# Kernel optimization log

Measured on AMD Instinct MI355X. Metric: run time of the kernel, lower is better.

The kernel has to match this reference:

```python
import jax, jax.numpy as jnp
import numpy as np

EPS = 1e-6
B, T, D = 8, 4096, 512


def setup_inputs() -> dict:
    key = jax.random.key(0)
    ks = jax.random.split(key, 8)
    s = 1.0 / np.sqrt(D)
    return {
        "summarization": jax.random.normal(ks[0], (B, D), jnp.float32),
        "decoder_output": jax.random.normal(ks[1], (B, T, D), jnp.float32),
        "W_hist": jax.random.normal(ks[2], (D, D), jnp.float32) * s,
        "b_hist": jnp.zeros((D,), jnp.float32),
        "W1": jax.random.normal(ks[3], (D, D), jnp.float32) * s,
        "W2": jax.random.normal(ks[4], (D, D), jnp.float32) * s,
        "W_out": jax.random.normal(ks[5], (D, D), jnp.float32) * s,
        "b_out": jnp.zeros((D,), jnp.float32),
        "gamma": jnp.ones((D,), jnp.float32),
        "beta": jnp.zeros((D,), jnp.float32),
    }


def reference(summarization, decoder_output, W_hist, b_hist, W1, W2, W_out, b_out, gamma, beta):
    # Causal running mean: equivalent to tril-mask bmm / row-count, but O(T).
    tgt_len = decoder_output.shape[1]
    counts = jnp.arange(1, tgt_len + 1, dtype=decoder_output.dtype)[None, :, None]
    history = jnp.cumsum(decoder_output, axis=1) / counts            # [B,T,D]
    history = jnp.tanh(history @ W_hist + b_hist)                    # history_linear + tanh
    # TransformMinus: linear1(summ) - linear2(history), then linear_out + tanh
    summ_proj = (summarization @ W1)[:, None, :]                     # [B,1,D] broadcasts over T
    out = summ_proj - history @ W2
    future = jnp.tanh(out @ W_out + b_out)
    # LayerPostprocessing (eval: dropout = identity): LayerNorm(future + decoder_output)
    x = future + decoder_output
    mu = jnp.mean(x, axis=-1, keepdims=True)
    var = jnp.mean(jnp.square(x - mu), axis=-1, keepdims=True)
    return (x - mu) / jnp.sqrt(var + EPS) * gamma + beta
```

## Files before the change

kernel.cpp:

```cpp
#include <hip/hip_runtime.h>
#include <hip/hip_bf16.h>
#include <stdint.h>
#include <stddef.h>

#define DEV static __device__ __forceinline__

typedef __attribute__((ext_vector_type(8))) short short8;
typedef __attribute__((ext_vector_type(4))) float floatx4;

constexpr int Tn = 4096, Dn = 512;
constexpr int NC = 128, CTm = 32;

union U8s { uint4 u4; unsigned short us[8]; };
union U4f { float4 f4; float f[4]; };
union U4s { uint2 u2; unsigned short us[4]; };

DEV float b2f(unsigned short u) {
  union { unsigned int i; float f; } c; c.i = ((unsigned int)u) << 16; return c.f;
}
DEV unsigned short f2b(float f) {
  union { float f; unsigned int u; } c; c.f = f;
  unsigned int r = c.u + 0x7fffu + ((c.u >> 16) & 1u);
  return (unsigned short)(r >> 16);
}
DEV float fast_tanh(float x) {
  float e = __expf(2.0f * x);
  return 1.0f - 2.0f / (e + 1.0f);
}

typedef __attribute__((address_space(1))) void GVOID;
typedef __attribute__((address_space(3))) void LVOID;
DEV void async16(const unsigned short* g, unsigned short* l) {
  __builtin_amdgcn_global_load_lds((GVOID*)g, (LVOID*)l, 16, 0, 0);
}

__global__ void k_scan_partial(const float* __restrict__ dec, float* __restrict__ part) {
  int idx = blockIdx.x * 256 + threadIdx.x;
  int d4 = idx & 127;
  int c  = (idx >> 7) & (NC - 1);
  int b  = idx >> 14;
  const float* p = dec + ((size_t)b * Tn + (size_t)c * CTm) * Dn + d4 * 4;
  float s[4] = {0,0,0,0};
#pragma unroll 4
  for (int i = 0; i < CTm; ++i) {
    U4f v; v.f4 = *(const float4*)(p + (size_t)i * Dn);
#pragma unroll
    for (int j = 0; j < 4; ++j) s[j] += v.f[j];
  }
  float* o = part + ((size_t)(b * NC + c)) * Dn + d4 * 4;
#pragma unroll
  for (int j = 0; j < 4; ++j) o[j] = s[j];
}

__global__ void k_scan_apply(const float* __restrict__ dec,
                             const float* __restrict__ part,
                             unsigned short* __restrict__ M) {
  int idx = blockIdx.x * 256 + threadIdx.x;
  int d8 = idx & 63;
  int c  = (idx >> 6) & (NC - 1);
  int b  = idx >> 13;
  size_t rbase = (size_t)b * Tn + (size_t)c * CTm;
  float s[8] = {0,0,0,0,0,0,0,0};
  const float* pb = part + (size_t)b * NC * Dn + d8 * 8;
  for (int cc = 0; cc < c; ++cc) {
    U4f p0, p1;
    p0.f4 = *(const float4*)(pb + (size_t)cc * Dn);
    p1.f4 = *(const float4*)(pb + (size_t)cc * Dn + 4);
#pragma unroll
    for (int j = 0; j < 4; ++j) { s[j] += p0.f[j]; s[j + 4] += p1.f[j]; }
  }
  int t0 = c * CTm;
  for (int i = 0; i < CTm; ++i) {
    U4f v0, v1; U8s o;
    v0.f4 = *(const float4*)(dec + (rbase + i) * Dn + d8 * 8);
    v1.f4 = *(const float4*)(dec + (rbase + i) * Dn + d8 * 8 + 4);
    float inv = 1.0f / (float)(t0 + i + 1);
#pragma unroll
    for (int j = 0; j < 4; ++j) {
      s[j] += v0.f[j];     o.us[j]     = f2b(s[j] * inv);
      s[j + 4] += v1.f[j]; o.us[j + 4] = f2b(s[j + 4] * inv);
    }
    *(uint4*)(M + (rbase + i) * Dn + d8 * 8) = o.u4;
  }
}

__global__ void k_svec(const float* __restrict__ summ,
                       const unsigned short* __restrict__ W1WoT,
                       const float* __restrict__ bo,
                       float* __restrict__ spo) {
  int widx = blockIdx.x * 4 + (threadIdx.x >> 6);
  int lane = threadIdx.x & 63;
  int n = widx & 511; int b = widx >> 9;
  U8s w8; w8.u4 = *(const uint4*)(W1WoT + (size_t)n * Dn + lane * 8);
  U4f s0, s1;
  s0.f4 = *(const float4*)(summ + (size_t)b * Dn + lane * 8);
  s1.f4 = *(const float4*)(summ + (size_t)b * Dn + lane * 8 + 4);
  float acc = 0.f;
#pragma unroll
  for (int j = 0; j < 4; ++j) acc += s0.f[j] * b2f(w8.us[j]);
#pragma unroll
  for (int j = 0; j < 4; ++j) acc += s1.f[j] * b2f(w8.us[j + 4]);
#pragma unroll
  for (int o = 32; o > 0; o >>= 1) acc += __shfl_xor(acc, o, 64);
  if (lane == 0) spo[(size_t)b * Dn + n] = acc + bo[n];
}

__global__ void k_wprep(const float* __restrict__ Wh, const float* __restrict__ Wo,
                        const float* __restrict__ W1, const float* __restrict__ W2,
                        unsigned short* __restrict__ WhT, unsigned short* __restrict__ WoT,
                        unsigned short* __restrict__ W1b, unsigned short* __restrict__ W2b) {
  int blk = blockIdx.x;
  if (blk < 128) {
    const float* in = (blk < 64) ? Wh : Wo;
    unsigned short* out = (blk < 64) ? WhT : WoT;
    int lb = blk & 63;
    __shared__ float t[64][65];
    int n0 = (lb & 7) * 64, k0 = (lb >> 3) * 64;
#pragma unroll
    for (int l = 0; l < 16; ++l) {
      int lin = l * 256 + threadIdx.x;
      int r = lin >> 6, c = lin & 63;
      t[r][c] = in[(size_t)(k0 + r) * 512 + n0 + c];
    }
    __syncthreads();
#pragma unroll
    for (int l = 0; l < 16; ++l) {
      int lin = l * 256 + threadIdx.x;
      int r = lin >> 6, c = lin & 63;
      out[(size_t)(n0 + r) * 512 + k0 + c] = f2b(t[c][r]);
    }
  } else {
    const float* in = (blk < 160) ? W1 : W2;
    unsigned short* out = (blk < 160) ? W1b : W2b;
    int lb = (blk - 128) & 31;
    size_t base = ((size_t)lb * 256 + threadIdx.x) * 32;
#pragma unroll
    for (int l = 0; l < 8; ++l) {
      U4f v; v.f4 = *(const float4*)(in + base + l * 4);
      U4s o;
#pragma unroll
      for (int j = 0; j < 4; ++j) o.us[j] = f2b(v.f[j]);
      *(uint2*)(out + base + l * 4) = o.u2;
    }
  }
}

template<int EPI>
DEV void gemm_core(const unsigned short* __restrict__ A, const unsigned short* __restrict__ BT,
                   unsigned short* __restrict__ C, const float* __restrict__ bias,
                   const float* __restrict__ sproj, int m0, int n0) {
  __shared__ alignas(16) unsigned short sA[128 * 64];
  __shared__ alignas(16) unsigned short sB[128 * 64];
  const int tid  = threadIdx.x;
  const int lane = tid & 63;
  const int w    = tid >> 6;
  const int wm   = (w >> 1) * 64;
  const int wn   = (w & 1) * 64;
  const int rs   = lane & 15;
  const int quad = lane >> 4;

  floatx4 acc[4][4];
#pragma unroll
  for (int i = 0; i < 4; ++i)
#pragma unroll
    for (int j = 0; j < 4; ++j) acc[i][j] = (floatx4){0.f, 0.f, 0.f, 0.f};

  for (int kt = 0; kt < 512; kt += 64) {
#pragma unroll
    for (int l = 0; l < 4; ++l) {
      int ch = l * 256 + tid;
      int r = ch >> 3, kc = ch & 7;
      async16(A  + (size_t)(m0 + r) * 512 + kt + kc * 8, sA + (size_t)ch * 8);
      async16(BT + (size_t)(n0 + r) * 512 + kt + kc * 8, sB + (size_t)ch * 8);
    }
    asm volatile("s_waitcnt vmcnt(0)" ::: "memory");
    __syncthreads();

#pragma unroll
    for (int kk = 0; kk < 2; ++kk) {
      const int kb = kk * 32 + quad * 8;
      short8 af[4], bfr[4];
#pragma unroll
      for (int i = 0; i < 4; ++i)
        af[i] = *(const short8*)(sA + (size_t)(wm + i * 16 + rs) * 64 + kb);
#pragma unroll
      for (int j = 0; j < 4; ++j)
        bfr[j] = *(const short8*)(sB + (size_t)(wn + j * 16 + rs) * 64 + kb);
#pragma unroll
      for (int i = 0; i < 4; ++i)
#pragma unroll
        for (int j = 0; j < 4; ++j)
          acc[i][j] = __builtin_amdgcn_mfma_f32_16x16x32_bf16(af[i], bfr[j], acc[i][j], 0, 0, 0);
    }
    __syncthreads();
  }

#pragma unroll
  for (int i = 0; i < 4; ++i) {
#pragma unroll
    for (int j = 0; j < 4; ++j) {
      const int colg = n0 + wn + j * 16 + rs;
#pragma unroll
      for (int r = 0; r < 4; ++r) {
        const int rowg = m0 + wm + i * 16 + quad * 4 + r;
        float v = acc[i][j][r];
        if constexpr (EPI == 0)      v = fast_tanh(v + bias[colg]);
        else if constexpr (EPI == 3) v = fast_tanh(sproj[(rowg >> 12) * Dn + colg] - v);
        C[(size_t)rowg * 512 + colg] = f2b(v);
      }
    }
  }
}

template<int EPI>
__global__ __launch_bounds__(256, 2)
void k_gemm(const unsigned short* __restrict__ A, const unsigned short* __restrict__ BT,
            unsigned short* __restrict__ C, const float* __restrict__ bias,
            const float* __restrict__ sproj) {
  gemm_core<EPI>(A, BT, C, bias, sproj, blockIdx.x * 128, blockIdx.y * 128);
}

__global__ __launch_bounds__(256, 2)
void k_wgemm(const unsigned short* __restrict__ WoT,
             const unsigned short* __restrict__ W2b, const unsigned short* __restrict__ W1b,
             unsigned short* __restrict__ W2WoT, unsigned short* __restrict__ W1WoT) {
  const unsigned short* BT = blockIdx.z ? W1b : W2b;
  unsigned short* C = blockIdx.z ? W1WoT : W2WoT;
  gemm_core<2>(WoT, BT, C, nullptr, nullptr, blockIdx.x * 128, blockIdx.y * 128);
}

__global__ void k_ln(const unsigned short* __restrict__ F, const float* __restrict__ dec,
                     const float* __restrict__ gamma, const float* __restrict__ beta,
                     float* __restrict__ out) {
  int row  = blockIdx.x * 4 + (threadIdx.x >> 6);
  int lane = threadIdx.x & 63;
  size_t base = (size_t)row * Dn + lane * 8;
  U8s f8; f8.u4 = *(const uint4*)(F + base);
  U4f d0, d1; d0.f4 = *(const float4*)(dec + base); d1.f4 = *(const float4*)(dec + base + 4);
  float x[8]; float s = 0.f, sq = 0.f;
#pragma unroll
  for (int j = 0; j < 8; ++j) {
    float dv = (j < 4) ? d0.f[j] : d1.f[j - 4];
    x[j] = b2f(f8.us[j]) + dv; s += x[j]; sq += x[j] * x[j];
  }
#pragma unroll
  for (int o = 32; o > 0; o >>= 1) { s += __shfl_xor(s, o, 64); sq += __shfl_xor(sq, o, 64); }
  float mu   = s * (1.0f / 512.0f);
  float var  = sq * (1.0f / 512.0f) - mu * mu;
  float rstd = rsqrtf(var + 1e-6f);
  U4f g0, g1, b0, b1, o0, o1;
  g0.f4 = *(const float4*)(gamma + lane * 8); g1.f4 = *(const float4*)(gamma + lane * 8 + 4);
  b0.f4 = *(const float4*)(beta  + lane * 8); b1.f4 = *(const float4*)(beta  + lane * 8 + 4);
#pragma unroll
  for (int j = 0; j < 8; ++j) {
    float g = (j < 4) ? g0.f[j] : g1.f[j - 4];
    float b = (j < 4) ? b0.f[j] : b1.f[j - 4];
    float v = (x[j] - mu) * rstd * g + b;
    if (j < 4) o0.f[j] = v; else o1.f[j - 4] = v;
  }
  *(float4*)(out + base) = o0.f4;
  *(float4*)(out + base + 4) = o1.f4;
}

extern "C" void kernel_launch(void* const* d_in, const int* in_sizes, int n_in,
                              void* d_out, int out_size, void* d_ws, size_t ws_size,
                              hipStream_t stream) {
  (void)in_sizes; (void)n_in; (void)out_size; (void)ws_size;
  const float* summ = (const float*)d_in[0];
  const float* dec  = (const float*)d_in[1];
  const float* Wh   = (const float*)d_in[2];
  const float* bh   = (const float*)d_in[3];
  const float* W1   = (const float*)d_in[4];
  const float* W2   = (const float*)d_in[5];
  const float* Wo   = (const float*)d_in[6];
  const float* bo   = (const float*)d_in[7];
  const float* gam  = (const float*)d_in[8];
  const float* bet  = (const float*)d_in[9];
  float* out = (float*)d_out;

  char* ws = (char*)d_ws;
  unsigned short* Mbuf  = (unsigned short*)(ws);
  unsigned short* Hbuf  = (unsigned short*)(ws + 33554432);
  float*          part  = (float*)(ws + 67108864);
  float*          spo   = (float*)(ws + 69206016);
  unsigned short* WhT   = (unsigned short*)(ws + 69238784);
  unsigned short* WoT   = (unsigned short*)(ws + 69763072);
  unsigned short* W2b   = (unsigned short*)(ws + 70287360);
  unsigned short* W2WoT = (unsigned short*)(ws + 70811648);
  unsigned short* W1b   = (unsigned short*)(ws + 71335936);
  unsigned short* W1WoT = (unsigned short*)(ws + 71860224);

  k_scan_partial<<<512, 256, 0, stream>>>(dec, part);

  k_wprep<<<192, 256, 0, stream>>>(Wh, Wo, W1, W2, WhT, WoT, W1b, W2b);
  k_wgemm<<<dim3(4, 4, 2), 256, 0, stream>>>(WoT, W2b, W1b, W2WoT, W1WoT);

  k_svec<<<1024, 256, 0, stream>>>(summ, W1WoT, bo, spo);

  k_scan_apply<<<256, 256, 0, stream>>>(dec, part, Mbuf);

  k_gemm<0><<<dim3(256, 4), 256, 0, stream>>>(Mbuf, WhT, Hbuf, bh, nullptr);
  k_gemm<3><<<dim3(256, 4), 256, 0, stream>>>(Hbuf, W2WoT, Mbuf, nullptr, spo);

  k_ln<<<8192, 256, 0, stream>>>(Mbuf, dec, gam, bet, out);
}
```

Baseline: 265.4 us.

## Fuse second GEMM with LayerNorm and add parallel chunk-prefix kernel for scan

The second GEMM now computes full 512-column rows per block (64x512 tile). Its epilogue applies tanh and the residual add, reduces mean and variance across waves through LDS, and writes the normalized fp32 output directly. This removes the separate LayerNorm kernel and the bf16 round-trip of the intermediate buffer. Separately, a new k_prefix kernel does an in-LDS Hillis-Steele scan of the chunk partial sums, so k_scan_apply reads one precomputed prefix instead of re-summing all earlier chunks, and it runs with more threads. The trade-off is that the fused GEMM uses a large (~72KB) LDS tile with no double buffering, which may limit occupancy and leave memory latency exposed.

```diff
diff --git a/kernel.cpp b/kernel.cpp
--- a/kernel.cpp
+++ b/kernel.cpp
@@ -52,35 +52,62 @@
   for (int j = 0; j < 4; ++j) o[j] = s[j];
 }
 
+__global__ void k_prefix(const float* __restrict__ part, float* __restrict__ P) {
+  int b = blockIdx.x >> 3, dg = blockIdx.x & 7;
+  __shared__ float S[NC * 64];
+  const float* src = part + (size_t)b * NC * Dn + dg * 64;
+#pragma unroll
+  for (int l = 0; l < 32; ++l) {
+    int lin = l * 256 + threadIdx.x;
+    int c = lin >> 6, d = lin & 63;
+    S[c * 64 + d] = src[(size_t)c * Dn + d];
+  }
+  __syncthreads();
+  for (int off = 1; off < NC; off <<= 1) {
+    float t[32];
+#pragma unroll
+    for (int l = 0; l < 32; ++l) {
+      int lin = l * 256 + threadIdx.x;
+      int c = lin >> 6, d = lin & 63;
+      t[l] = (c >= off) ? S[(c - off) * 64 + d] : 0.f;
+    }
+    __syncthreads();
+#pragma unroll
+    for (int l = 0; l < 32; ++l) {
+      int lin = l * 256 + threadIdx.x;
+      int c = lin >> 6, d = lin & 63;
+      S[c * 64 + d] += t[l];
+    }
+    __syncthreads();
+  }
+  float* dst = P + (size_t)b * NC * Dn + dg * 64;
+#pragma unroll
+  for (int l = 0; l < 32; ++l) {
+    int lin = l * 256 + threadIdx.x;
+    int c = lin >> 6, d = lin & 63;
+    dst[(size_t)c * Dn + d] = (c > 0) ? S[(c - 1) * 64 + d] : 0.f;
+  }
+}
+
 __global__ void k_scan_apply(const float* __restrict__ dec,
-                             const float* __restrict__ part,
+                             const float* __restrict__ P,
                              unsigned short* __restrict__ M) {
   int idx = blockIdx.x * 256 + threadIdx.x;
-  int d8 = idx & 63;
-  int c  = (idx >> 6) & (NC - 1);
-  int b  = idx >> 13;
+  int d4 = idx & 127;
+  int c  = (idx >> 7) & (NC - 1);
+  int b  = idx >> 14;
   size_t rbase = (size_t)b * Tn + (size_t)c * CTm;
-  float s[8] = {0,0,0,0,0,0,0,0};
-  const float* pb = part + (size_t)b * NC * Dn + d8 * 8;
-  for (int cc = 0; cc < c; ++cc) {
-    U4f p0, p1;
-    p0.f4 = *(const float4*)(pb + (size_t)cc * Dn);
-    p1.f4 = *(const float4*)(pb + (size_t)cc * Dn + 4);
-#pragma unroll
-    for (int j = 0; j < 4; ++j) { s[j] += p0.f[j]; s[j + 4] += p1.f[j]; }
-  }
+  U4f pv; pv.f4 = *(const float4*)(P + ((size_t)(b * NC + c)) * Dn + d4 * 4);
+  float s[4] = {pv.f[0], pv.f[1], pv.f[2], pv.f[3]};
   int t0 = c * CTm;
+#pragma unroll 4
   for (int i = 0; i < CTm; ++i) {
-    U4f v0, v1; U8s o;
-    v0.f4 = *(const float4*)(dec + (rbase + i) * Dn + d8 * 8);
-    v1.f4 = *(const float4*)(dec + (rbase + i) * Dn + d8 * 8 + 4);
+    U4f v; v.f4 = *(const float4*)(dec + (rbase + i) * Dn + d4 * 4);
+    U4s o;
     float inv = 1.0f / (float)(t0 + i + 1);
 #pragma unroll
-    for (int j = 0; j < 4; ++j) {
-      s[j] += v0.f[j];     o.us[j]     = f2b(s[j] * inv);
-      s[j + 4] += v1.f[j]; o.us[j + 4] = f2b(s[j + 4] * inv);
-    }
-    *(uint4*)(M + (rbase + i) * Dn + d8 * 8) = o.u4;
+    for (int j = 0; j < 4; ++j) { s[j] += v.f[j]; o.us[j] = f2b(s[j] * inv); }
+    *(uint2*)(M + (rbase + i) * Dn + d4 * 4) = o.u2;
   }
 }
 
@@ -148,7 +175,7 @@
 template<int EPI>
 DEV void gemm_core(const unsigned short* __restrict__ A, const unsigned short* __restrict__ BT,
                    unsigned short* __restrict__ C, const float* __restrict__ bias,
-                   const float* __restrict__ sproj, int m0, int n0) {
+                   int m0, int n0) {
   __shared__ alignas(16) unsigned short sA[128 * 64];
   __shared__ alignas(16) unsigned short sB[128 * 64];
   const int tid  = threadIdx.x;
@@ -204,8 +231,7 @@
       for (int r = 0; r < 4; ++r) {
         const int rowg = m0 + wm + i * 16 + quad * 4 + r;
         float v = acc[i][j][r];
-        if constexpr (EPI == 0)      v = fast_tanh(v + bias[colg]);
-        else if constexpr (EPI == 3) v = fast_tanh(sproj[(rowg >> 12) * Dn + colg] - v);
+        if constexpr (EPI == 0) v = fast_tanh(v + bias[colg]);
         C[(size_t)rowg * 512 + colg] = f2b(v);
       }
     }
@@ -215,9 +241,8 @@
 template<int EPI>
 __global__ __launch_bounds__(256, 2)
 void k_gemm(const unsigned short* __restrict__ A, const unsigned short* __restrict__ BT,
-            unsigned short* __restrict__ C, const float* __restrict__ bias,
-            const float* __restrict__ sproj) {
-  gemm_core<EPI>(A, BT, C, bias, sproj, blockIdx.x * 128, blockIdx.y * 128);
+            unsigned short* __restrict__ C, const float* __restrict__ bias) {
+  gemm_core<EPI>(A, BT, C, bias, blockIdx.x * 128, blockIdx.y * 128);
 }
 
 __global__ __launch_bounds__(256, 2)
@@ -226,40 +251,138 @@
              unsigned short* __restrict__ W2WoT, unsigned short* __restrict__ W1WoT) {
   const unsigned short* BT = blockIdx.z ? W1b : W2b;
   unsigned short* C = blockIdx.z ? W1WoT : W2WoT;
-  gemm_core<2>(WoT, BT, C, nullptr, nullptr, blockIdx.x * 128, blockIdx.y * 128);
-}
-
-__global__ void k_ln(const unsigned short* __restrict__ F, const float* __restrict__ dec,
-                     const float* __restrict__ gamma, const float* __restrict__ beta,
-                     float* __restrict__ out) {
-  int row  = blockIdx.x * 4 + (threadIdx.x >> 6);
-  int lane = threadIdx.x & 63;
-  size_t base = (size_t)row * Dn + lane * 8;
-  U8s f8; f8.u4 = *(const uint4*)(F + base);
-  U4f d0, d1; d0.f4 = *(const float4*)(dec + base); d1.f4 = *(const float4*)(dec + base + 4);
-  float x[8]; float s = 0.f, sq = 0.f;
-#pragma unroll
-  for (int j = 0; j < 8; ++j) {
-    float dv = (j < 4) ? d0.f[j] : d1.f[j - 4];
-    x[j] = b2f(f8.us[j]) + dv; s += x[j]; sq += x[j] * x[j];
-  }
-#pragma unroll
-  for (int o = 32; o > 0; o >>= 1) { s += __shfl_xor(s, o, 64); sq += __shfl_xor(sq, o, 64); }
-  float mu   = s * (1.0f / 512.0f);
-  float var  = sq * (1.0f / 512.0f) - mu * mu;
-  float rstd = rsqrtf(var + 1e-6f);
-  U4f g0, g1, b0, b1, o0, o1;
-  g0.f4 = *(const float4*)(gamma + lane * 8); g1.f4 = *(const float4*)(gamma + lane * 8 + 4);
-  b0.f4 = *(const float4*)(beta  + lane * 8); b1.f4 = *(const float4*)(beta  + lane * 8 + 4);
-#pragma unroll
-  for (int j = 0; j < 8; ++j) {
-    float g = (j < 4) ? g0.f[j] : g1.f[j - 4];
-    float b = (j < 4) ? b0.f[j] : b1.f[j - 4];
-    float v = (x[j] - mu) * rstd * g + b;
-    if (j < 4) o0.f[j] = v; else o1.f[j - 4] = v;
-  }
-  *(float4*)(out + base) = o0.f4;
-  *(float4*)(out + base + 4) = o1.f4;
+  gemm_core<2>(WoT, BT, C, nullptr, blockIdx.x * 128, blockIdx.y * 128);
+}
+
+__global__ __launch_bounds__(512, 4)
+void k_gemm2ln(const unsigned short* __restrict__ H, const unsigned short* __restrict__ BT,
+               const float* __restrict__ spo, const float* __restrict__ dec,
+               const float* __restrict__ gamma, const float* __restrict__ beta,
+               float* __restrict__ out) {
+  __shared__ alignas(16) unsigned short sA[64 * 64];
+  __shared__ alignas(16) unsigned short sB[512 * 64];
+  const int tid  = threadIdx.x;
+  const int lane = tid & 63;
+  const int cg   = tid >> 6;
+  const int m0   = blockIdx.x * 64;
+  const int b    = blockIdx.x >> 6;
+  const int rs   = lane & 15;
+  const int quad = lane >> 4;
+
+  floatx4 acc[4][4];
+#pragma unroll
+  for (int i = 0; i < 4; ++i)
+#pragma unroll
+    for (int j = 0; j < 4; ++j) acc[i][j] = (floatx4){0.f, 0.f, 0.f, 0.f};
+
+  for (int kt = 0; kt < 512; kt += 64) {
+    {
+      int r = tid >> 3, kc = tid & 7;
+      async16(H + (size_t)(m0 + r) * 512 + kt + kc * 8, sA + (size_t)tid * 8);
+    }
+#pragma unroll
+    for (int l = 0; l < 8; ++l) {
+      int ch = l * 512 + tid;
+      int r = ch >> 3, kc = ch & 7;
+      async16(BT + (size_t)r * 512 + kt + kc * 8, sB + (size_t)ch * 8);
+    }
+    asm volatile("s_waitcnt vmcnt(0)" ::: "memory");
+    __syncthreads();
+
+#pragma unroll
+    for (int kk = 0; kk < 2; ++kk) {
+      const int kb = kk * 32 + quad * 8;
+      short8 af[4], bfr[4];
+#pragma unroll
+      for (int i = 0; i < 4; ++i)
+        af[i] = *(const short8*)(sA + (size_t)(i * 16 + rs) * 64 + kb);
+#pragma unroll
+      for (int j = 0; j < 4; ++j)
+        bfr[j] = *(const short8*)(sB + (size_t)(cg * 64 + j * 16 + rs) * 64 + kb);
+#pragma unroll
+      for (int i = 0; i < 4; ++i)
+#pragma unroll
+        for (int j = 0; j < 4; ++j)
+          acc[i][j] = __builtin_amdgcn_mfma_f32_16x16x32_bf16(af[i], bfr[j], acc[i][j], 0, 0, 0);
+    }
+    __syncthreads();
+  }
+
+  float* redS = (float*)sA;
+  float* redQ = redS + 512;
+  float* muL  = redQ + 512;
+  float* rsL  = muL + 64;
+
+  float spo_v[4], gam_v[4], bet_v[4];
+#pragma unroll
+  for (int j = 0; j < 4; ++j) {
+    int col = cg * 64 + j * 16 + rs;
+    spo_v[j] = spo[(size_t)b * 512 + col];
+    gam_v[j] = gamma[col];
+    bet_v[j] = beta[col];
+  }
+
+  float ps[4][4], ps2[4][4];
+#pragma unroll
+  for (int i = 0; i < 4; ++i)
+#pragma unroll
+    for (int r = 0; r < 4; ++r) { ps[i][r] = 0.f; ps2[i][r] = 0.f; }
+
+#pragma unroll
+  for (int i = 0; i < 4; ++i)
+#pragma unroll
+    for (int j = 0; j < 4; ++j) {
+      const int colg = cg * 64 + j * 16 + rs;
+#pragma unroll
+      for (int r = 0; r < 4; ++r) {
+        const int rowg = m0 + i * 16 + quad * 4 + r;
+        float x = fast_tanh(spo_v[j] - acc[i][j][r]) + dec[(size_t)rowg * 512 + colg];
+        acc[i][j][r] = x;
+        ps[i][r] += x; ps2[i][r] += x * x;
+      }
+    }
+#pragma unroll
+  for (int off = 1; off < 16; off <<= 1)
+#pragma unroll
+    for (int i = 0; i < 4; ++i)
+#pragma unroll
+      for (int r = 0; r < 4; ++r) {
+        ps[i][r]  += __shfl_xor(ps[i][r],  off, 64);
+        ps2[i][r] += __shfl_xor(ps2[i][r], off, 64);
+      }
+  if (rs == 0) {
+#pragma unroll
+    for (int i = 0; i < 4; ++i)
+#pragma unroll
+      for (int r = 0; r < 4; ++r) {
+        int rl = i * 16 + quad * 4 + r;
+        redS[rl * 8 + cg] = ps[i][r];
+        redQ[rl * 8 + cg] = ps2[i][r];
+      }
+  }
+  __syncthreads();
+  if (tid < 64) {
+    float s = 0.f, q = 0.f;
+#pragma unroll
+    for (int g = 0; g < 8; ++g) { s += redS[tid * 8 + g]; q += redQ[tid * 8 + g]; }
+    float mu = s * (1.0f / 512.0f);
+    float var = q * (1.0f / 512.0f) - mu * mu;
+    muL[tid] = mu;
+    rsL[tid] = rsqrtf(var + 1e-6f);
+  }
+  __syncthreads();
+#pragma unroll
+  for (int i = 0; i < 4; ++i)
+#pragma unroll
+    for (int r = 0; r < 4; ++r) {
+      int rl = i * 16 + quad * 4 + r;
+      float mu = muL[rl], rstd = rsL[rl];
+#pragma unroll
+      for (int j = 0; j < 4; ++j) {
+        int colg = cg * 64 + j * 16 + rs;
+        out[(size_t)(m0 + rl) * 512 + colg] = (acc[i][j][r] - mu) * rstd * gam_v[j] + bet_v[j];
+      }
+    }
 }
 
 extern "C" void kernel_launch(void* const* d_in, const int* in_sizes, int n_in,
@@ -281,6 +404,7 @@
   char* ws = (char*)d_ws;
   unsigned short* Mbuf  = (unsigned short*)(ws);
   unsigned short* Hbuf  = (unsigned short*)(ws + 33554432);
+  float*          pfix  = (float*)(ws + 33554432);
   float*          part  = (float*)(ws + 67108864);
   float*          spo   = (float*)(ws + 69206016);
   unsigned short* WhT   = (unsigned short*)(ws + 69238784);
@@ -294,13 +418,11 @@
 
   k_wprep<<<192, 256, 0, stream>>>(Wh, Wo, W1, W2, WhT, WoT, W1b, W2b);
   k_wgemm<<<dim3(4, 4, 2), 256, 0, stream>>>(WoT, W2b, W1b, W2WoT, W1WoT);
-
   k_svec<<<1024, 256, 0, stream>>>(summ, W1WoT, bo, spo);
 
-  k_scan_apply<<<256, 256, 0, stream>>>(dec, part, Mbuf);
-
-  k_gemm<0><<<dim3(256, 4), 256, 0, stream>>>(Mbuf, WhT, Hbuf, bh, nullptr);
-  k_gemm<3><<<dim3(256, 4), 256, 0, stream>>>(Hbuf, W2WoT, Mbuf, nullptr, spo);
-
-  k_ln<<<8192, 256, 0, stream>>>(Mbuf, dec, gam, bet, out);
-}
+  k_prefix<<<64, 256, 0, stream>>>(part, pfix);
+  k_scan_apply<<<512, 256, 0, stream>>>(dec, pfix, Mbuf);
+
+  k_gemm<0><<<dim3(256, 4), 256, 0, stream>>>(Mbuf, WhT, Hbuf, bh);
+  k_gemm2ln<<<512, 512, 0, stream>>>(Hbuf, W2WoT, spo, dec, gam, bet, out);
+}
```

Result: slower. 313.7 us (+18.2%).
